# Kernel optimization log

Hardware: AMD Instinct MI355X
Metric: run time of the kernel (lower is better)

The kernel has to match this reference:

```python
import jax, jax.numpy as jnp
import numpy as np

TWO_THIRDS = 2.0 / 3.0
SEVENTEEN_SIXTHS = 17.0 / 6.0


def _grid():
    # torch: cat(-flip(logspace(-2,2,100)**2), [0], logspace(-2,2,100)**2) -> 201 points
    gp = jnp.logspace(-2.0, 2.0, 100, dtype=jnp.float32) ** 2
    return jnp.concatenate([-gp[::-1], jnp.zeros((1,), jnp.float32), gp])


def _trapz_w(x):
    # trapezoidal quadrature weights so that trapz(f, x) == sum(f * w)
    dx = jnp.diff(x)
    w = jnp.zeros_like(x)
    return w.at[:-1].add(0.5 * dx).at[1:].add(0.5 * dx)


def setup_inputs() -> dict:
    key = jax.random.key(0)
    k1k, kyk, kzk = jax.random.split(key, 3)
    k1 = jnp.sort(jax.random.uniform(k1k, (512,), jnp.float32, 0.01, 1.0))  # positive wavenumbers
    dy = jax.random.uniform(kyk, (64,), jnp.float32, 0.0, 50.0)  # spanwise separations [m]
    dz = jax.random.uniform(kzk, (64,), jnp.float32, 0.0, 50.0)  # vertical separations [m]
    return {
        "k1_input": k1,
        "Delta_y": dy,
        "Delta_z": dz,
        "logLengthScale": jnp.float32(np.log(0.7 * 42.0)),
        "logTimeScale": jnp.float32(np.log(3.9)),
        "logMagnitude": jnp.float32(0.0),
    }


def reference(k1_input, Delta_y, Delta_z, logLengthScale, logTimeScale, logMagnitude):
    L = jnp.exp(logLengthScale)
    T = jnpp = jnp.exp(logTimeScale)
    M = jnp.exp(logMagnitude)
    k2g = _grid()  # [201]
    k3g = _grid()  # [201]
    # broadcasted meshgrid (never materialize a 4D stacked k tensor)
    k1 = k1_input[:, None, None]   # [Nk1,1,1]
    k2 = k2g[None, :, None]        # [1,201,1]
    k3 = k3g[None, None, :]        # [1,1,201]
    kk = k1 * k1 + k2 * k2 + k3 * k3
    # EddyLifetime 'TwoThird': beta = T * (L*|k|)^{-2/3}
    beta = T * (L * jnp.sqrt(kk)) ** (-TWO_THIRDS)
    k30 = k3 + beta * k1
    kk0 = k1 * k1 + k2 * k2 + k30 * k30
    k0L = L * jnp.sqrt(kk0)
    # von Karman energy spectrum at distorted wavevector
    E0 = M * k0L ** 4 / (1.0 + k0L * k0L) ** SEVENTEEN_SIXTHS
    # RDT spectral tensor, 11-component (module uses Phi[0] for Phi11, Phi33 and Phi13)
    s = k1 * k1 + k2 * k2
    C1 = beta * k1 * k1 * (kk0 - 2.0 * k30 * k30 + beta * k1 * k30) / (kk * s)
    C2 = k2 * kk0 / s ** 1.5 * jnp.arctan2(beta * k1 * jnp.sqrt(s), kk0 - k30 * k1 * beta)
    zeta1 = C1 - (k2 / k1) * C2
    Phi11 = E0 / (4.0 * jnp.pi * kk0 * kk0) * (
        kk0 - k1 * k1 - 2.0 * k1 * k30 * zeta1 + s * zeta1 * zeta1
    )  # [Nk1,201,201]
    # double trapezoid over (k2,k3) as weighted sums
    w2 = _trapz_w(k2g)
    w3 = _trapz_w(k3g)
    F1 = jnp.einsum('aij,i,j->a', Phi11, w2, w3)  # = F3
    den = jnp.sqrt(F1 * F1)
    # exp(i(k2*dy + k3*dz)) is separable -> factor the nested loop into two einsums
    Pw = (Phi11 * w2[None, :, None] * w3[None, None, :]).astype(jnp.complex64)
    E3 = jnp.exp(1j * k3g[:, None] * Delta_z[None, :])  # [201,Nz]
    E2 = jnp.exp(1j * k2g[:, None] * Delta_y[None, :])  # [201,Ny]
    A = jnp.einsum('aij,jz->aiz', Pw, E3)   # [Nk1,201,Nz]
    I = jnp.einsum('aiz,iy->ayz', A, E2)    # [Nk1,Ny,Nz]
    return jnp.real(I) / den[:, None, None]
```

## Files before the change

kernel.cpp:

```cpp
#include <hip/hip_runtime.h>
#include <math.h>

#define BLOCK 512
#define LOG2_10 3.3219280948873623f
#define PI_F 3.14159265358979f
#define INV2PI 0.15915494309189535f
#define PW_SCALE 256.0f

#define SP 128
#define SA 128
#define FT 56

typedef _Float16 half8 __attribute__((ext_vector_type(8)));
typedef _Float16 half2v __attribute__((ext_vector_type(2)));
typedef float f32x4 __attribute__((ext_vector_type(4)));
typedef float v2f  __attribute__((ext_vector_type(2)));
typedef int   i32x4 __attribute__((ext_vector_type(4)));

__device__ __forceinline__ v2f v2(float a, float b) { v2f r; r.x = a; r.y = b; return r; }

__device__ __forceinline__ float fast_cos(float x_rev) {
    return __builtin_amdgcn_cosf(__builtin_amdgcn_fractf(x_rev));
}

__device__ __forceinline__ v2f atan2_pos_pk(float yv, v2f x) {
    float ax0 = __builtin_fabsf(x.x), ax1 = __builtin_fabsf(x.y);
    float mn0 = fminf(ax0, yv), mx0 = fmaxf(ax0, yv);
    float mn1 = fminf(ax1, yv), mx1 = fmaxf(ax1, yv);
    v2f a = v2(mn0 * __builtin_amdgcn_rcpf(mx0), mn1 * __builtin_amdgcn_rcpf(mx1));
    v2f t = a * a;
    v2f p = ((((( -0.0117212f * t + 0.05265332f) * t - 0.11643287f) * t
              + 0.19354346f) * t - 0.33262347f) * t + 0.99997726f) * a;
    float p0 = (yv > ax0) ? (1.57079632679f - p.x) : p.x;
    float p1 = (yv > ax1) ? (1.57079632679f - p.y) : p.y;
    p0 = (x.x < 0.0f) ? (3.14159265359f - p0) : p0;
    p1 = (x.y < 0.0f) ? (3.14159265359f - p1) : p1;
    return v2(p0, p1);
}

__device__ __forceinline__ float phi_pair_pk(float k1, float k1sq, float n2k1, float Ttk1,
                                             float L2, float s, float sqs, float k2sc, float g) {
    const float kk  = g * g + s;
    const float bk1 = Ttk1 * __builtin_amdgcn_exp2f((-1.0f/3.0f) * __builtin_amdgcn_logf(L2 * kk));
    const float Qh  = bk1 * g;
    const float sg  = 2.0f * s - kk;
    const float cc  = (bk1 * k1) * __builtin_amdgcn_rcpf(kk * s);
    const float yv  = bk1 * sqs;
    const float R   = bk1 * bk1 + kk;
    const v2f x   = v2(kk - Qh, kk + Qh);
    const v2f C1  = cc * v2(sg + Qh, sg - Qh);
    const v2f kk0 = v2(R - 2.0f * Qh, R + 2.0f * Qh);
    const v2f th  = atan2_pos_pk(yv, x);
    const v2f vv  = L2 * kk0 + 1.0f;
    const v2f p   = v2(__builtin_amdgcn_exp2f((-17.0f/6.0f) * __builtin_amdgcn_logf(vv.x)),
                       __builtin_amdgcn_exp2f((-17.0f/6.0f) * __builtin_amdgcn_logf(vv.y)));
    const v2f z   = C1 - k2sc * (kk0 * th);
    const v2f k30 = v2(bk1 - g, bk1 + g);
    const v2f qq  = (s * z + n2k1 * k30) * z + (kk0 - k1sq);
    const v2f r   = p * qq;
    return r.x + r.y;
}

__device__ __forceinline__ float phi_pair_cheap(float k1sq, float L2, float s, float g) {
    const float kk = g * g + s;
    const float p  = __builtin_amdgcn_exp2f((-17.0f/6.0f) *
                     __builtin_amdgcn_logf(fmaf(L2, kk, 1.0f)));
    return 2.0f * p * (kk - k1sq);
}

__global__ __launch_bounds__(BLOCK, 2)
void spectral_kernel(const float* __restrict__ k1_in,
                     const float* __restrict__ dy_in,
                     const float* __restrict__ dz_in,
                     const float* __restrict__ plogL,
                     const float* __restrict__ plogT,
                     const float* __restrict__ plogM,
                     float* __restrict__ out)
{
    __shared__ __attribute__((aligned(16))) _Float16 s_phiT[2 * 2 * 32 * SP];
    __shared__ __attribute__((aligned(16))) _Float16 s_B3T[64 * SP];
    __shared__ __attribute__((aligned(16))) _Float16 s_A2[64 * SA];
    __shared__ float  s_grid[204];
    __shared__ float2 s_gw[204];
    __shared__ float  s_dy[64], s_dz[64];
    __shared__ float  s_redA[8], s_redB[8], s_rden[2];

    const int t    = threadIdx.x;
    const int a0   = blockIdx.x * 2;
    const int lane = t & 63;
    const int w    = t >> 6;
    const int n16  = lane & 15;
    const int quad = lane >> 4;

    const float L  = expf(plogL[0]);
    const float Tt = expf(plogT[0]);
    const float M  = expf(plogM[0]);
    const float L2 = L * L;
    const float L4 = L2 * L2;
    const float k1A   = k1_in[a0];
    const float k1B   = k1_in[a0 + 1];
    const float k1sqA = k1A * k1A,  k1sqB = k1B * k1B;
    const float n2k1A = -2.0f * k1A, n2k1B = -2.0f * k1B;
    const float Ttk1A = Tt * k1A,    Ttk1B = Tt * k1B;
    const float rk1A  = __builtin_amdgcn_rcpf(k1A);
    const float rk1B  = __builtin_amdgcn_rcpf(k1B);
    const float cM0   = (M * 0.25f / PI_F) * PW_SCALE * L4;

    if (t < 204) {
        int tt = min(t, 200);
        float v;
        if (tt < 100)       v = -exp2f(LOG2_10 * (-4.0f + 8.0f * (float)(99 - tt) * (1.0f/99.0f)));
        else if (tt == 100) v = 0.0f;
        else                v =  exp2f(LOG2_10 * (-4.0f + 8.0f * (float)(tt - 101) * (1.0f/99.0f)));
        s_grid[t] = v;
    }
    if (t < 64) { s_dy[t] = dy_in[t]; s_dz[t] = dz_in[t]; }
    __syncthreads();

    if (t < 204) {
        float wv = 0.0f;
        if (t == 0)          wv = 0.5f * (s_grid[1] - s_grid[0]);
        else if (t < 200)    wv = 0.5f * (s_grid[t+1] - s_grid[t-1]);
        else if (t == 200)   wv = 0.5f * (s_grid[200] - s_grid[199]);
        s_gw[t] = make_float2(s_grid[t], wv);
    }
    {
        const int jjp = lane;
        const int jj0 = 2 * jjp, jj1 = jj0 + 1;
        if (jj0 < 96) {
            const float g0 = s_grid[100 + jj0];
            const float g1 = s_grid[100 + jj1];
            const int jjg  = jjp >> 2;
            #pragma unroll
            for (int m = 0; m < 8; ++m) {
                int z = w + 8 * m;
                float dzr = s_dz[z] * INV2PI;
                float c0 = (jj0 < 88) ? fast_cos(g0 * dzr) : 0.0f;
                float c1 = (jj1 < 88) ? fast_cos(g1 * dzr) : 0.0f;
                half2v pr; pr.x = (_Float16)c0; pr.y = (_Float16)c1;
                *(half2v*)&s_B3T[z * SP + ((jjg ^ (z & 7)) << 3) + (jj0 & 7)] = pr;
            }
        }
    }
    {
        float dyr = s_dy[lane] * INV2PI;
        #pragma unroll
        for (int k = 0; k < 6; ++k) {
            int iip = w + 8 * k;
            int i0 = 2 * iip, i1 = i0 + 1;
            float c0 = (i0 < 88) ? fast_cos(s_grid[100 + i0] * dyr) : 0.0f;
            float c1 = (i1 < 88) ? fast_cos(s_grid[100 + i1] * dyr) : 0.0f;
            half2v pr; pr.x = (_Float16)c0; pr.y = (_Float16)c1;
            int off = lane * SA + (((iip >> 2) ^ (lane & 7)) << 3) + ((iip & 3) << 1);
            *(half2v*)&s_A2[off] = pr;
        }
    }
    __syncthreads();

    float f1A = 0.0f, f1B = 0.0f;
    f32x4 acc2[4];
    #pragma unroll
    for (int i = 0; i < 4; ++i) acc2[i] = (f32x4){0.f, 0.f, 0.f, 0.f};

    auto do_full2 = [&](int ii, int jj, int row, _Float16* bp0, _Float16* bp1) {
        float k2  = s_gw[100 + ii].x;
        float cMw = cM0 * (s_gw[100 + ii].y * ((ii == 0) ? 1.0f : 2.0f));
        float2 gwv = s_gw[100 + jj];
        float cw  = cMw * ((jj == 0) ? 0.5f * gwv.y : gwv.y);
        float sA   = k1sqA + k2 * k2;
        float rsA  = __builtin_amdgcn_rsqf(sA);
        float valA = phi_pair_pk(k1A, k1sqA, n2k1A, Ttk1A, L2, sA, sA * rsA,
                                 (k2 * rk1A) * k2 * (rsA * rsA * rsA), gwv.x) * cw;
        float sB   = k1sqB + k2 * k2;
        float rsB  = __builtin_amdgcn_rsqf(sB);
        float valB = phi_pair_pk(k1B, k1sqB, n2k1B, Ttk1B, L2, sB, sB * rsB,
                                 (k2 * rk1B) * k2 * (rsB * rsB * rsB), gwv.x) * cw;
        f1A += valA; f1B += valB;
        int off = row * SP + (((jj >> 3) ^ (row & 7)) << 3) + (jj & 7);
        bp0[off] = (_Float16)valA;
        bp1[off] = (_Float16)valB;
    };
    auto do_cheap2 = [&](int ii, int jj, int row, _Float16* bp0, _Float16* bp1) {
        float k2  = s_gw[100 + ii].x;
        float cMw = cM0 * (s_gw[100 + ii].y * ((ii == 0) ? 1.0f : 2.0f));
        float2 gwv = s_gw[100 + jj];
        float cw  = cMw * ((jj == 0) ? 0.5f * gwv.y : gwv.y);
        float valA = phi_pair_cheap(k1sqA, L2, k1sqA + k2 * k2, gwv.x) * cw;
        float valB = phi_pair_cheap(k1sqB, L2, k1sqB + k2 * k2, gwv.x) * cw;
        f1A += valA; f1B += valB;
        int off = row * SP + (((jj >> 3) ^ (row & 7)) << 3) + (jj & 7);
        bp0[off] = (_Float16)valA;
        bp1[off] = (_Float16)valB;
    };

    _Float16* pA0 = s_phiT;
    _Float16* pA1 = s_phiT + 32 * SP;
    _Float16* pB0 = s_phiT + 64 * SP;
    _Float16* pB1 = s_phiT + 96 * SP;

    {
        if (t < 32) {
            half8 zz = {};
            int off = t * SP + ((11 ^ (t & 7)) << 3);
            *(half8*)&pA0[off] = zz;
            *(half8*)&pB0[off] = zz;
        }
        #pragma unroll
        for (int m = 0; m < 4; ++m) {
            int e = t + 512 * m;
            if (e < 1792) {
                int row = e / FT, jj = e - row * FT;
                do_full2(row, jj, row, pA0, pB0);
            }
        }
        #pragma unroll
        for (int m = 0; m < 2; ++m) {
            int e = t + 512 * m;
            int row = e >> 5, jj = FT + (e & 31);
            do_cheap2(row, jj, row, pA0, pB0);
        }
    }
    __syncthreads();

    const int ia = w >> 2;
    const int zb = w & 3;
    const float* k1sel = ia ? &k1B : &k1A;

    for (int c = 0; c < 3; ++c) {
        const _Float16* rp = s_phiT + ia * (64 * SP) + (c & 1) * (32 * SP);

        f32x4 acc1[2];
        acc1[0] = (f32x4){0.f,0.f,0.f,0.f};
        acc1[1] = (f32x4){0.f,0.f,0.f,0.f};
        {
            const int arow0 = n16;
            const int arow1 = 16 + n16;
            const int brow  = zb * 16 + n16;
            #pragma unroll
            for (int ks = 0; ks < 3; ++ks) {
                int kg = ks * 4 + quad;
                half8 af0 = *(const half8*)&rp[arow0 * SP + ((kg ^ (arow0 & 7)) << 3)];
                half8 af1 = *(const half8*)&rp[arow1 * SP + ((kg ^ (arow1 & 7)) << 3)];
                half8 bf  = *(const half8*)&s_B3T[brow * SP + ((kg ^ (brow & 7)) << 3)];
                acc1[0] = __builtin_amdgcn_mfma_f32_16x16x32_f16(af0, bf, acc1[0], 0, 0, 0);
                acc1[1] = __builtin_amdgcn_mfma_f32_16x16x32_f16(af1, bf, acc1[1], 0, 0, 0);
            }
        }

        half8 bf2;
        {
            half2v hA0; hA0.x = (_Float16)acc1[0].x; hA0.y = (_Float16)acc1[0].y;
            half2v hA1; hA1.x = (_Float16)acc1[0].z; hA1.y = (_Float16)acc1[0].w;
            half2v hB0; hB0.x = (_Float16)acc1[1].x; hB0.y = (_Float16)acc1[1].y;
            half2v hB1; hB1.x = (_Float16)acc1[1].z; hB1.y = (_Float16)acc1[1].w;
            int pkA0 = __builtin_bit_cast(int, hA0);
            int pkA1 = __builtin_bit_cast(int, hA1);
            int pkB0 = __builtin_bit_cast(int, hB0);
            int pkB1 = __builtin_bit_cast(int, hB1);
            const int addr_a = (((quad & 1) << 5) + n16) << 2;
            const int addr_b = addr_a + 64;
            int a0v = __builtin_amdgcn_ds_bpermute(addr_a, pkA0);
            int b0v = __builtin_amdgcn_ds_bpermute(addr_a, pkB0);
            int a1v = __builtin_amdgcn_ds_bpermute(addr_a, pkA1);
            int b1v = __builtin_amdgcn_ds_bpermute(addr_a, pkB1);
            int a2v = __builtin_amdgcn_ds_bpermute(addr_b, pkA0);
            int b2v = __builtin_amdgcn_ds_bpermute(addr_b, pkB0);
            int a3v = __builtin_amdgcn_ds_bpermute(addr_b, pkA1);
            int b3v = __builtin_amdgcn_ds_bpermute(addr_b, pkB1);
            const bool lo = (quad < 2);
            i32x4 wv;
            wv.x = lo ? a0v : b0v;
            wv.y = lo ? a1v : b1v;
            wv.z = lo ? a2v : b2v;
            wv.w = lo ? a3v : b3v;
            bf2 = __builtin_bit_cast(half8, wv);
        }

        {
            const int G = c * 4 + quad;
            #pragma unroll
            for (int yb = 0; yb < 4; ++yb) {
                int yrow = yb * 16 + n16;
                half8 a2f = *(const half8*)&s_A2[yrow * SA + ((G ^ (yrow & 7)) << 3)];
                acc2[yb] = __builtin_amdgcn_mfma_f32_16x16x32_f16(a2f, bf2, acc2[yb], 0, 0, 0);
            }
        }

        if (c == 0) {
            if (t < 32) {
                half8 zz = {};
                int off = t * SP + ((11 ^ (t & 7)) << 3);
                *(half8*)&pA1[off] = zz;
                *(half8*)&pB1[off] = zz;
            }
            #pragma unroll
            for (int m = 0; m < 3; ++m) {
                int e = t + 512 * m;
                if (e < 1344) {
                    int row = e / FT, jj = e - row * FT;
                    do_full2(32 + row, jj, row, pA1, pB1);
                }
            }
            #pragma unroll
            for (int m = 0; m < 3; ++m) {
                int e = t + 512 * m;
                if (e < 1472) {
                    int row, jj;
                    if (e < 768) { row = e >> 5; jj = FT + (e & 31); }
                    else { int e2 = e - 768; row = 24 + e2 / 88; jj = e2 - (row - 24) * 88; }
                    do_cheap2(32 + row, jj, row, pA1, pB1);
                }
            }
        } else if (c == 1) {
            if (t < 120) {
                int row, slot;
                if (t < 96) { row = 24 + t / 12; int g = t - (row - 24) * 12; slot = g ^ (row & 7); }
                else        { row = t - 96;      slot = 11 ^ (row & 7); }
                half8 zz = {};
                *(half8*)&pA0[row * SP + (slot << 3)] = zz;
                *(half8*)&pB0[row * SP + (slot << 3)] = zz;
            }
            #pragma unroll
            for (int m = 0; m < 5; ++m) {
                int e = t + 512 * m;
                if (e < 2112) {
                    int row = e / 88, jj = e - row * 88;
                    do_cheap2(64 + row, jj, row, pA0, pB0);
                }
            }
        }
        __syncthreads();
    }

    float vA = f1A, vB = f1B;
    #pragma unroll
    for (int off = 32; off > 0; off >>= 1) {
        vA += __shfl_down(vA, off, 64);
        vB += __shfl_down(vB, off, 64);
    }
    if (lane == 0) { s_redA[w] = vA; s_redB[w] = vB; }
    __syncthreads();
    if (t == 0) {
        float sA = 0.0f, sB = 0.0f;
        #pragma unroll
        for (int i = 0; i < 8; ++i) { sA += s_redA[i]; sB += s_redB[i]; }
        s_rden[0] = 1.0f / fabsf(sA);
        s_rden[1] = 1.0f / fabsf(sB);
    }
    __syncthreads();
    const float rden = s_rden[ia];

    float* op = out + ((size_t)(a0 + ia) << 12) + (zb * 16 + n16);
    #pragma unroll
    for (int yb = 0; yb < 4; ++yb) {
        #pragma unroll
        for (int r = 0; r < 4; ++r) {
            int y = yb * 16 + quad * 4 + r;
            op[y * 64] = acc2[yb][r] * rden;
        }
    }
    (void)k1sel;
}

extern "C" void kernel_launch(void* const* d_in, const int* in_sizes, int n_in,
                              void* d_out, int out_size, void* d_ws, size_t ws_size,
                              hipStream_t stream) {
    const float* k1 = (const float*)d_in[0];
    const float* dy = (const float*)d_in[1];
    const float* dz = (const float*)d_in[2];
    const float* lL = (const float*)d_in[3];
    const float* lT = (const float*)d_in[4];
    const float* lM = (const float*)d_in[5];
    float* outp = (float*)d_out;
    hipLaunchKernelGGL(spectral_kernel, dim3(256), dim3(BLOCK), 0, stream,
                       k1, dy, dz, lL, lT, lM, outp);
}
```

Before: 75.69 us.

## Drop double-buffered phi tile and generate each chunk just before its MFMA pass

Replaces the double-buffered phi staging with a single buffer. Each of the three k2 chunks is now generated in a generic loop, followed by a barrier and then the MFMA passes, instead of computing the next chunk while the current one is consumed. Several loops are set to unroll 1, which cuts LDS use and code size and is probably meant to lower register pressure. In exchange it gives up the overlap between phi generation and matrix work and adds an extra barrier per chunk.

```diff
diff --git a/kernel.cpp b/kernel.cpp
--- a/kernel.cpp
+++ b/kernel.cpp
@@ -77,7 +77,7 @@
                      const float* __restrict__ plogM,
                      float* __restrict__ out)
 {
-    __shared__ __attribute__((aligned(16))) _Float16 s_phiT[2 * 2 * 32 * SP];
+    __shared__ __attribute__((aligned(16))) _Float16 s_phiT[2 * 32 * SP];
     __shared__ __attribute__((aligned(16))) _Float16 s_B3T[64 * SP];
     __shared__ __attribute__((aligned(16))) _Float16 s_A2[64 * SA];
     __shared__ float  s_grid[204];
@@ -131,7 +131,7 @@
             const float g0 = s_grid[100 + jj0];
             const float g1 = s_grid[100 + jj1];
             const int jjg  = jjp >> 2;
-            #pragma unroll
+            #pragma unroll 1
             for (int m = 0; m < 8; ++m) {
                 int z = w + 8 * m;
                 float dzr = s_dz[z] * INV2PI;
@@ -144,7 +144,7 @@
     }
     {
         float dyr = s_dy[lane] * INV2PI;
-        #pragma unroll
+        #pragma unroll 1
         for (int k = 0; k < 6; ++k) {
             int iip = w + 8 * k;
             int i0 = 2 * iip, i1 = i0 + 1;
@@ -162,73 +162,88 @@
     #pragma unroll
     for (int i = 0; i < 4; ++i) acc2[i] = (f32x4){0.f, 0.f, 0.f, 0.f};
 
-    auto do_full2 = [&](int ii, int jj, int row, _Float16* bp0, _Float16* bp1) {
-        float k2  = s_gw[100 + ii].x;
-        float cMw = cM0 * (s_gw[100 + ii].y * ((ii == 0) ? 1.0f : 2.0f));
-        float2 gwv = s_gw[100 + jj];
-        float cw  = cMw * ((jj == 0) ? 0.5f * gwv.y : gwv.y);
-        float sA   = k1sqA + k2 * k2;
-        float rsA  = __builtin_amdgcn_rsqf(sA);
-        float valA = phi_pair_pk(k1A, k1sqA, n2k1A, Ttk1A, L2, sA, sA * rsA,
-                                 (k2 * rk1A) * k2 * (rsA * rsA * rsA), gwv.x) * cw;
-        float sB   = k1sqB + k2 * k2;
-        float rsB  = __builtin_amdgcn_rsqf(sB);
-        float valB = phi_pair_pk(k1B, k1sqB, n2k1B, Ttk1B, L2, sB, sB * rsB,
-                                 (k2 * rk1B) * k2 * (rsB * rsB * rsB), gwv.x) * cw;
-        f1A += valA; f1B += valB;
-        int off = row * SP + (((jj >> 3) ^ (row & 7)) << 3) + (jj & 7);
-        bp0[off] = (_Float16)valA;
-        bp1[off] = (_Float16)valB;
-    };
-    auto do_cheap2 = [&](int ii, int jj, int row, _Float16* bp0, _Float16* bp1) {
-        float k2  = s_gw[100 + ii].x;
-        float cMw = cM0 * (s_gw[100 + ii].y * ((ii == 0) ? 1.0f : 2.0f));
-        float2 gwv = s_gw[100 + jj];
-        float cw  = cMw * ((jj == 0) ? 0.5f * gwv.y : gwv.y);
-        float valA = phi_pair_cheap(k1sqA, L2, k1sqA + k2 * k2, gwv.x) * cw;
-        float valB = phi_pair_cheap(k1sqB, L2, k1sqB + k2 * k2, gwv.x) * cw;
-        f1A += valA; f1B += valB;
-        int off = row * SP + (((jj >> 3) ^ (row & 7)) << 3) + (jj & 7);
-        bp0[off] = (_Float16)valA;
-        bp1[off] = (_Float16)valB;
-    };
-
-    _Float16* pA0 = s_phiT;
-    _Float16* pA1 = s_phiT + 32 * SP;
-    _Float16* pB0 = s_phiT + 64 * SP;
-    _Float16* pB1 = s_phiT + 96 * SP;
-
-    {
+    _Float16* pA = s_phiT;
+    _Float16* pB = s_phiT + 32 * SP;
+    const int ia = w >> 2;
+    const int zb = w & 3;
+
+    for (int c = 0; c < 3; ++c) {
+        const int Rf  = (c == 0) ? 32 : ((c == 1) ? 24 : 0);
+        const int R   = (c == 2) ? 24 : 32;
+        const int iiB = c * 32;
+
         if (t < 32) {
             half8 zz = {};
             int off = t * SP + ((11 ^ (t & 7)) << 3);
-            *(half8*)&pA0[off] = zz;
-            *(half8*)&pB0[off] = zz;
-        }
-        #pragma unroll
-        for (int m = 0; m < 4; ++m) {
-            int e = t + 512 * m;
-            if (e < 1792) {
-                int row = e / FT, jj = e - row * FT;
-                do_full2(row, jj, row, pA0, pB0);
-            }
-        }
-        #pragma unroll
-        for (int m = 0; m < 2; ++m) {
-            int e = t + 512 * m;
+            *(half8*)&pA[off] = zz;
+            *(half8*)&pB[off] = zz;
+        }
+        if (c == 2 && t < 96) {
+            int row = 24 + t / 12, g = t - (row - 24) * 12;
+            half8 zz = {};
+            int off = row * SP + ((g ^ (row & 7)) << 3);
+            *(half8*)&pA[off] = zz;
+            *(half8*)&pB[off] = zz;
+        }
+
+        const int Nf = Rf * FT;
+        #pragma unroll 1
+        for (int e = t; e < Nf; e += BLOCK) {
+            int row = e / FT, jj = e - row * FT;
+            int ii  = iiB + row;
+            float k2  = s_gw[100 + ii].x;
+            float cMw = cM0 * (s_gw[100 + ii].y * ((ii == 0) ? 1.0f : 2.0f));
+            float2 gwv = s_gw[100 + jj];
+            float cw  = cMw * ((jj == 0) ? 0.5f * gwv.y : gwv.y);
+            float sA   = k1sqA + k2 * k2;
+            float rsA  = __builtin_amdgcn_rsqf(sA);
+            float valA = phi_pair_pk(k1A, k1sqA, n2k1A, Ttk1A, L2, sA, sA * rsA,
+                                     (k2 * rk1A) * k2 * (rsA * rsA * rsA), gwv.x) * cw;
+            float sB   = k1sqB + k2 * k2;
+            float rsB  = __builtin_amdgcn_rsqf(sB);
+            float valB = phi_pair_pk(k1B, k1sqB, n2k1B, Ttk1B, L2, sB, sB * rsB,
+                                     (k2 * rk1B) * k2 * (rsB * rsB * rsB), gwv.x) * cw;
+            f1A += valA; f1B += valB;
+            int off = row * SP + (((jj >> 3) ^ (row & 7)) << 3) + (jj & 7);
+            pA[off] = (_Float16)valA;
+            pB[off] = (_Float16)valB;
+        }
+        const int N1 = R * 32;
+        #pragma unroll 1
+        for (int e = t; e < N1; e += BLOCK) {
             int row = e >> 5, jj = FT + (e & 31);
-            do_cheap2(row, jj, row, pA0, pB0);
-        }
-    }
-    __syncthreads();
-
-    const int ia = w >> 2;
-    const int zb = w & 3;
-    const float* k1sel = ia ? &k1B : &k1A;
-
-    for (int c = 0; c < 3; ++c) {
-        const _Float16* rp = s_phiT + ia * (64 * SP) + (c & 1) * (32 * SP);
-
+            int ii  = iiB + row;
+            float k2  = s_gw[100 + ii].x;
+            float cMw = cM0 * (s_gw[100 + ii].y * ((ii == 0) ? 1.0f : 2.0f));
+            float2 gwv = s_gw[100 + jj];
+            float cw  = cMw * gwv.y;
+            float valA = phi_pair_cheap(k1sqA, L2, k1sqA + k2 * k2, gwv.x) * cw;
+            float valB = phi_pair_cheap(k1sqB, L2, k1sqB + k2 * k2, gwv.x) * cw;
+            f1A += valA; f1B += valB;
+            int off = row * SP + (((jj >> 3) ^ (row & 7)) << 3) + (jj & 7);
+            pA[off] = (_Float16)valA;
+            pB[off] = (_Float16)valB;
+        }
+        const int N2 = (R - Rf) * FT;
+        #pragma unroll 1
+        for (int e = t; e < N2; e += BLOCK) {
+            int r2 = e / FT, jj = e - r2 * FT;
+            int row = Rf + r2;
+            int ii  = iiB + row;
+            float k2  = s_gw[100 + ii].x;
+            float cMw = cM0 * (s_gw[100 + ii].y * 2.0f);
+            float2 gwv = s_gw[100 + jj];
+            float cw  = cMw * ((jj == 0) ? 0.5f * gwv.y : gwv.y);
+            float valA = phi_pair_cheap(k1sqA, L2, k1sqA + k2 * k2, gwv.x) * cw;
+            float valB = phi_pair_cheap(k1sqB, L2, k1sqB + k2 * k2, gwv.x) * cw;
+            f1A += valA; f1B += valB;
+            int off = row * SP + (((jj >> 3) ^ (row & 7)) << 3) + (jj & 7);
+            pA[off] = (_Float16)valA;
+            pB[off] = (_Float16)valB;
+        }
+        __syncthreads();
+
+        const _Float16* rp = s_phiT + ia * (32 * SP);
         f32x4 acc1[2];
         acc1[0] = (f32x4){0.f,0.f,0.f,0.f};
         acc1[1] = (f32x4){0.f,0.f,0.f,0.f};
@@ -285,50 +300,6 @@
                 acc2[yb] = __builtin_amdgcn_mfma_f32_16x16x32_f16(a2f, bf2, acc2[yb], 0, 0, 0);
             }
         }
-
-        if (c == 0) {
-            if (t < 32) {
-                half8 zz = {};
-                int off = t * SP + ((11 ^ (t & 7)) << 3);
-                *(half8*)&pA1[off] = zz;
-                *(half8*)&pB1[off] = zz;
-            }
-            #pragma unroll
-            for (int m = 0; m < 3; ++m) {
-                int e = t + 512 * m;
-                if (e < 1344) {
-                    int row = e / FT, jj = e - row * FT;
-                    do_full2(32 + row, jj, row, pA1, pB1);
-                }
-            }
-            #pragma unroll
-            for (int m = 0; m < 3; ++m) {
-                int e = t + 512 * m;
-                if (e < 1472) {
-                    int row, jj;
-                    if (e < 768) { row = e >> 5; jj = FT + (e & 31); }
-                    else { int e2 = e - 768; row = 24 + e2 / 88; jj = e2 - (row - 24) * 88; }
-                    do_cheap2(32 + row, jj, row, pA1, pB1);
-                }
-            }
-        } else if (c == 1) {
-            if (t < 120) {
-                int row, slot;
-                if (t < 96) { row = 24 + t / 12; int g = t - (row - 24) * 12; slot = g ^ (row & 7); }
-                else        { row = t - 96;      slot = 11 ^ (row & 7); }
-                half8 zz = {};
-                *(half8*)&pA0[row * SP + (slot << 3)] = zz;
-                *(half8*)&pB0[row * SP + (slot << 3)] = zz;
-            }
-            #pragma unroll
-            for (int m = 0; m < 5; ++m) {
-                int e = t + 512 * m;
-                if (e < 2112) {
-                    int row = e / 88, jj = e - row * 88;
-                    do_cheap2(64 + row, jj, row, pA0, pB0);
-                }
-            }
-        }
         __syncthreads();
     }
 
@@ -359,7 +330,6 @@
             op[y * 64] = acc2[yb][r] * rden;
         }
     }
-    (void)k1sel;
 }
 
 extern "C" void kernel_launch(void* const* d_in, const int* in_sizes, int n_in,
```

Measured after the change: 79.21 us. +4.7%, slower.
